# Kernel optimization log

Hardware: AMD Instinct MI355X
Metric: run time of the kernel (lower is better)

The kernel has to match this reference:

```python
import jax, jax.numpy as jnp
import numpy as np

B, T, D = 8, 2048, 1024   # batch, seq_len (== block_size), n_embed
HS = 128                   # head_size

def setup_inputs() -> dict:
    key = jax.random.key(0)
    kx, kk, kq, kv = jax.random.split(key, 4)
    s = D ** -0.5  # torch Linear default init scale ~ U(-1/sqrt(in), 1/sqrt(in))
    x  = jax.random.normal(kx, (B, T, D), dtype=jnp.float32)
    Wk = jax.random.uniform(kk, (HS, D), jnp.float32, -s, s)
    Wq = jax.random.uniform(kq, (HS, D), jnp.float32, -s, s)
    Wv = jax.random.uniform(kv, (HS, D), jnp.float32, -s, s)
    return {"x": x, "Wk": Wk, "Wq": Wq, "Wv": Wv}

def reference(x, Wk, Wq, Wv):
    # single-head causal self-attention; dropout disabled (eval mode)
    Tlen = x.shape[1]
    k = jnp.einsum('btd,hd->bth', x, Wk)   # [B,T,HS]
    q = jnp.einsum('btd,hd->bth', x, Wq)
    v = jnp.einsum('btd,hd->bth', x, Wv)
    scale = Wk.shape[0] ** -0.5
    scores = jnp.einsum('bth,bsh->bts', q, k) * scale   # [B,T,T]
    causal = jnp.tril(jnp.ones((Tlen, Tlen), dtype=bool))
    scores = jnp.where(causal, scores, -jnp.inf)
    weights = jax.nn.softmax(scores, axis=-1)
    out = jnp.einsum('bts,bsh->bth', weights, v)        # [B,T,HS]
    return out
```

## Files before the change

### kernel.cpp

```cpp
#include <hip/hip_runtime.h>
#include <hip/hip_bf16.h>
#include <math.h>

#define BATCH_N 8
#define SEQ_T   2048
#define DIM_D   1024
#define HS_N    128

using bf16x8_t = __attribute__((ext_vector_type(8))) __bf16;
using bf16x4_t = __attribute__((ext_vector_type(4))) __bf16;
using f32x4_t  = __attribute__((ext_vector_type(4))) float;

__device__ __forceinline__ f32x4_t mfma_16x16x32(bf16x8_t a, bf16x8_t b, f32x4_t c) {
  return __builtin_amdgcn_mfma_f32_16x16x32_bf16(a, b, c, 0, 0, 0);
}

__device__ __forceinline__ void async_cp16(const void* g, void* l) {
  __builtin_amdgcn_global_load_lds(
      (const __attribute__((address_space(1))) unsigned int*)g,
      (__attribute__((address_space(3))) unsigned int*)l, 16, 0, 0);
}

#define BAR()      __builtin_amdgcn_s_barrier()
#define FENCE()    asm volatile("" ::: "memory")
#define WAIT_VM(n) asm volatile("s_waitcnt vmcnt(" #n ")" ::: "memory")
#define WAIT_LGKM0 asm volatile("s_waitcnt lgkmcnt(0)" ::: "memory")

__global__ __launch_bounds__(256) void castw_kernel(
    const float* __restrict__ Wk, const float* __restrict__ Wq,
    const float* __restrict__ Wv, __bf16* __restrict__ Wb,
    unsigned int* __restrict__ km) {
  if (blockIdx.x == 0 && threadIdx.x < 8) km[threadIdx.x] = 0u;
  int idx = blockIdx.x * 256 + threadIdx.x;
  int e   = idx * 4;
  int row = e >> 10;
  int col = e & 1023;
  const float* src;
  float sc = 1.0f;
  if (row < 128) {
    src = Wk + row * DIM_D + col;
  } else if (row < 256) {
    src = Wq + (row - 128) * DIM_D + col;
    sc  = 0.08838834764831845f;
  } else {
    src = Wv + (row - 256) * DIM_D + col;
  }
  float4 v = *(const float4*)src;
  bf16x4_t o;
  o[0] = (__bf16)(v.x * sc); o[1] = (__bf16)(v.y * sc);
  o[2] = (__bf16)(v.z * sc); o[3] = (__bf16)(v.w * sc);
  *(bf16x4_t*)(Wb + e) = o;
}

__global__ __launch_bounds__(512, 2) void proj_kernel(
    const float* __restrict__ x, const __bf16* __restrict__ Wb,
    __bf16* __restrict__ Qb, __bf16* __restrict__ Kb, __bf16* __restrict__ Vt,
    unsigned int* __restrict__ km) {
  __shared__ __align__(16) char psmem[65536];

  const int tid  = threadIdx.x;
  const int lane = tid & 63;
  const int wave = tid >> 6;
  const int h    = wave >> 2;
  const int g    = wave & 3;
  const int lr = lane & 15;
  const int lq = lane >> 4;
  const int m0 = blockIdx.x * 64;

  f32x4_t acc[2][6];
  #pragma unroll
  for (int mt = 0; mt < 2; ++mt)
    #pragma unroll
    for (int nt = 0; nt < 6; ++nt) acc[mt][nt] = (f32x4_t){0.f, 0.f, 0.f, 0.f};

  auto stageA = [&](int kt) {
    char* As = psmem + (kt & 1) * 8192;
    const int r = wave * 8 + (lane >> 3);
    const int c = (lane & 7) ^ ((lane >> 3) & 7);
    async_cp16(x + (size_t)(m0 + r) * DIM_D + kt * 32 + c * 4,
               As + wave * 1024);
  };

  auto stageB = [&](int kt) {
    __bf16* Bs = (__bf16*)(psmem + 16384 + (kt & 1) * 24576);
    #pragma unroll
    for (int c = wave; c < 24; c += 8) {
      const int row = c * 16 + (lane >> 2);
      const int u   = (lane & 3) ^ ((row >> 1) & 3);
      async_cp16(Wb + (size_t)row * DIM_D + kt * 32 + u * 8, Bs + c * 512);
    }
  };

  stageA(0);
  stageB(0);

  for (int kt = 0; kt < 32; ++kt) {
    if (kt + 1 < 32) {
      stageA(kt + 1);
      stageB(kt + 1);
      WAIT_VM(4);
    } else {
      WAIT_VM(0);
    }
    BAR();
    FENCE();

    const float*  As = (const float*)(psmem + (kt & 1) * 8192);
    const __bf16* Bs = (const __bf16*)(psmem + 16384 + (kt & 1) * 24576);

    bf16x8_t af[2];
    #pragma unroll
    for (int mt = 0; mt < 2; ++mt) {
      const int ml = h * 32 + mt * 16 + lr;
      const int u0 = (lq * 2)     ^ (ml & 7);
      const int u1 = (lq * 2 + 1) ^ (ml & 7);
      f32x4_t lo = *(const f32x4_t*)(As + ml * 32 + u0 * 4);
      f32x4_t hi = *(const f32x4_t*)(As + ml * 32 + u1 * 4);
      bf16x8_t a;
      a[0] = (__bf16)lo[0]; a[1] = (__bf16)lo[1];
      a[2] = (__bf16)lo[2]; a[3] = (__bf16)lo[3];
      a[4] = (__bf16)hi[0]; a[5] = (__bf16)hi[1];
      a[6] = (__bf16)hi[2]; a[7] = (__bf16)hi[3];
      af[mt] = a;
    }
    bf16x8_t bfv[6];
    #pragma unroll
    for (int nt = 0; nt < 6; ++nt) {
      const int nl = g * 96 + nt * 16 + lr;
      bfv[nt] = *(const bf16x8_t*)(&Bs[nl * 32 + ((lq ^ ((nl >> 1) & 3)) * 8)]);
    }
    #pragma unroll
    for (int mt = 0; mt < 2; ++mt)
      #pragma unroll
      for (int nt = 0; nt < 6; ++nt)
        acc[mt][nt] = mfma_16x16x32(af[mt], bfv[nt], acc[mt][nt]);
    WAIT_LGKM0;
    BAR();
    FENCE();
  }

  __syncthreads();
  float* rowss = (float*)psmem;
  if (tid < 64) rowss[tid] = 0.f;
  __syncthreads();
  if (g < 2) {
    #pragma unroll
    for (int mt = 0; mt < 2; ++mt)
      #pragma unroll
      for (int r = 0; r < 4; ++r) {
        float s = 0.f;
        #pragma unroll
        for (int nt = 0; nt < 6; ++nt)
          if (g == 0 || nt < 2) s += acc[mt][nt][r] * acc[mt][nt][r];
        s += __shfl_xor(s, 1); s += __shfl_xor(s, 2);
        s += __shfl_xor(s, 4); s += __shfl_xor(s, 8);
        if (lr == 0) atomicAdd(&rowss[h * 32 + mt * 16 + lq * 4 + r], s);
      }
  }
  __syncthreads();
  if (tid < 64) {
    float v = rowss[tid];
    #pragma unroll
    for (int off = 1; off < 64; off <<= 1) v = fmaxf(v, __shfl_xor(v, off));
    if (tid == 0) atomicMax(km + (m0 >> 11), __float_as_uint(v));
  }

  #pragma unroll
  for (int mt = 0; mt < 2; ++mt) {
    const int t0 = m0 + h * 32 + mt * 16 + lq * 4;
    #pragma unroll
    for (int nt = 0; nt < 6; ++nt) {
      const int nn = g * 96 + nt * 16 + lr;
      if (nn < 256) {
        __bf16* dst = (nn < 128) ? (Kb + nn) : (Qb + (nn - 128));
        #pragma unroll
        for (int r = 0; r < 4; ++r)
          dst[(size_t)(t0 + r) * HS_N] = (__bf16)acc[mt][nt][r];
      } else {
        const int bb = t0 >> 11;
        const int tl = t0 & 2047;
        bf16x4_t o;
        #pragma unroll
        for (int r = 0; r < 4; ++r) o[r] = (__bf16)acc[mt][nt][r];
        *(bf16x4_t*)(Vt + (size_t)bb * (HS_N * SEQ_T) + (size_t)(nn - 256) * SEQ_T + tl) = o;
      }
    }
  }
}

__global__ __launch_bounds__(256, 2) void attn_kernel(
    const __bf16* __restrict__ Qb, const __bf16* __restrict__ Kb,
    const __bf16* __restrict__ Vt, const unsigned int* __restrict__ km,
    __bf16* __restrict__ Opart, float* __restrict__ lpart) {
  __shared__ __align__(16) char smem[81920];
  __bf16* KsBase = (__bf16*)smem;
  __bf16* VsBase = (__bf16*)(smem + 32768);
  float*  Ofl    = (float*)smem;

  const int lane = threadIdx.x & 63;
  const int wave = threadIdx.x >> 6;
  const int lr = lane & 15;
  const int lq = lane >> 4;
  const int bid  = blockIdx.x;
  const int b    = bid & 7;
  const int rest = bid >> 3;
  const int jg   = 15 - (rest >> 2);
  const int p4   = rest & 3;
  const int Q0   = jg * 128;
  const int qa   = Q0 + wave * 32;
  const int ch   = 2 * (jg + 1);
  const int c0   = (p4 * ch) >> 2;
  const int c1   = ((p4 + 1) * ch) >> 2;

  const __bf16* Qbb = Qb + (size_t)b * (SEQ_T * HS_N);
  const __bf16* Kbb = Kb + (size_t)b * (SEQ_T * HS_N);
  const __bf16* Vbb = Vt + (size_t)b * (HS_N * SEQ_T);
  __bf16* pbA = (__bf16*)(smem + 65536 + wave * 4096);
  __bf16* pbB = (__bf16*)(smem + 65536 + wave * 4096 + 2048);

  bf16x8_t qf[2][4];
  #pragma unroll
  for (int t = 0; t < 2; ++t)
    #pragma unroll
    for (int ks = 0; ks < 4; ++ks)
      qf[t][ks] = *(const bf16x8_t*)(Qbb + (size_t)(qa + t * 16 + lr) * HS_N
                                     + ks * 32 + lq * 8);

  const float km2 = __uint_as_float(km[b]);
  float mrow[2][4];
  #pragma unroll
  for (int t = 0; t < 2; ++t) {
    float qn2 = 0.f;
    #pragma unroll
    for (int ks = 0; ks < 4; ++ks)
      #pragma unroll
      for (int j = 0; j < 8; ++j) { float f = (float)qf[t][ks][j]; qn2 += f * f; }
    qn2 += __shfl_xor(qn2, 16);
    qn2 += __shfl_xor(qn2, 32);
    #pragma unroll
    for (int r2 = 0; r2 < 4; ++r2)
      mrow[t][r2] = sqrtf(__shfl(qn2, lq * 4 + r2) * km2);
  }

  f32x4_t Oa[2][8];
  #pragma unroll
  for (int t = 0; t < 2; ++t)
    #pragma unroll
    for (int o = 0; o < 8; ++o) Oa[t][o] = (f32x4_t){0.f, 0.f, 0.f, 0.f};
  float lsum[2][4] = {{0.f,0.f,0.f,0.f},{0.f,0.f,0.f,0.f}};

  auto stage = [&](int bufi, int c) {
    const int kk = c * 64;
    __bf16* Ks = KsBase + bufi * 8192;
    for (int idx = wave; idx < 32; idx += 4) {
      if (idx < 16) {
        const int row = idx * 4 + (lane >> 4);
        const int u   = (lane & 15) ^ (row & 15);
        async_cp16(Kbb + (size_t)(kk + row) * HS_N + u * 8, Ks + idx * 512);
      } else {
        const int i2  = idx - 16;
        const int row = i2 * 8 + (lane >> 3);
        const int u   = (lane & 7) ^ (row & 7);
        async_cp16(Vbb + (size_t)row * SEQ_T + kk + u * 8, VsBase + bufi * 8192 + i2 * 512);
      }
    }
  };

  if (c0 < c1) stage(0, c0);
  __syncthreads();

  for (int c = c0; c < c1; ++c) {
    const int cur = (c - c0) & 1;
    if (c + 1 < c1) {
      stage(cur ^ 1, c + 1);
      WAIT_VM(8);
    } else {
      WAIT_VM(0);
    }
    BAR();
    FENCE();

    const int kk = c * 64;
    const __bf16* Ks = KsBase + cur * 8192;
    const __bf16* Vs = VsBase + cur * 8192;

    f32x4_t s0[4], s1[4];
    #pragma unroll
    for (int nt = 0; nt < 4; ++nt) {
      s0[nt] = (f32x4_t){0.f, 0.f, 0.f, 0.f};
      s1[nt] = (f32x4_t){0.f, 0.f, 0.f, 0.f};
    }
    #pragma unroll
    for (int ks = 0; ks < 4; ++ks)
      #pragma unroll
      for (int nt = 0; nt < 4; ++nt) {
        bf16x8_t kf = *(const bf16x8_t*)(
            &Ks[(nt * 16 + lr) * 128 + (((ks * 4 + lq) ^ lr) * 8)]);
        s0[nt] = mfma_16x16x32(qf[0][ks], kf, s0[nt]);
        s1[nt] = mfma_16x16x32(qf[1][ks], kf, s1[nt]);
      }
    const int q0a = qa, q0b = qa + 16;
    if (kk + 63 > q0a) {
      #pragma unroll
      for (int nt = 0; nt < 4; ++nt) {
        const int col = kk + nt * 16 + lr;
        #pragma unroll
        for (int r2 = 0; r2 < 4; ++r2)
          if (col > q0a + lq * 4 + r2) s0[nt][r2] = -INFINITY;
      }
    }
    if (kk + 63 > q0b) {
      #pragma unroll
      for (int nt = 0; nt < 4; ++nt) {
        const int col = kk + nt * 16 + lr;
        #pragma unroll
        for (int r2 = 0; r2 < 4; ++r2)
          if (col > q0b + lq * 4 + r2) s1[nt][r2] = -INFINITY;
      }
    }

    #pragma unroll
    for (int r2 = 0; r2 < 4; ++r2) {
      float a0 = __expf(s0[0][r2] - mrow[0][r2]);
      float a1 = __expf(s0[1][r2] - mrow[0][r2]);
      float a2 = __expf(s0[2][r2] - mrow[0][r2]);
      float a3 = __expf(s0[3][r2] - mrow[0][r2]);
      s0[0][r2] = a0; s0[1][r2] = a1; s0[2][r2] = a2; s0[3][r2] = a3;
      lsum[0][r2] += (a0 + a1) + (a2 + a3);
      float b0 = __expf(s1[0][r2] - mrow[1][r2]);
      float b1 = __expf(s1[1][r2] - mrow[1][r2]);
      float b2 = __expf(s1[2][r2] - mrow[1][r2]);
      float b3 = __expf(s1[3][r2] - mrow[1][r2]);
      s1[0][r2] = b0; s1[1][r2] = b1; s1[2][r2] = b2; s1[3][r2] = b3;
      lsum[1][r2] += (b0 + b1) + (b2 + b3);
    }

    #pragma unroll
    for (int nt = 0; nt < 4; ++nt)
      #pragma unroll
      for (int r2 = 0; r2 < 4; ++r2) {
        const int prow = lq * 4 + r2;
        const int pcol = (nt * 16 + lr) ^ ((prow & 7) << 3);
        pbA[prow * 64 + pcol] = (__bf16)s0[nt][r2];
        pbB[prow * 64 + pcol] = (__bf16)s1[nt][r2];
      }

    #pragma unroll
    for (int k2 = 0; k2 < 2; ++k2) {
      const int au = ((k2 * 4 + lq) ^ (lr & 7)) << 3;
      bf16x8_t afrA = *(const bf16x8_t*)(pbA + lr * 64 + au);
      bf16x8_t afrB = *(const bf16x8_t*)(pbB + lr * 64 + au);
      #pragma unroll
      for (int o = 0; o < 8; ++o) {
        bf16x8_t vfr = *(const bf16x8_t*)(
            &Vs[(o * 16 + lr) * 64 + (((k2 * 4 + lq) ^ (lr & 7)) * 8)]);
        Oa[0][o] = mfma_16x16x32(afrA, vfr, Oa[0][o]);
        Oa[1][o] = mfma_16x16x32(afrB, vfr, Oa[1][o]);
      }
    }
    WAIT_LGKM0;
    BAR();
    FENCE();
  }

  #pragma unroll
  for (int t = 0; t < 2; ++t)
    #pragma unroll
    for (int r2 = 0; r2 < 4; ++r2) {
      float v = lsum[t][r2];
      v += __shfl_xor(v, 1);
      v += __shfl_xor(v, 2);
      v += __shfl_xor(v, 4);
      v += __shfl_xor(v, 8);
      if (lr == 0)
        lpart[bid * 128 + wave * 32 + t * 16 + lq * 4 + r2] = v;
    }

  #pragma unroll
  for (int t = 0; t < 2; ++t)
    #pragma unroll
    for (int o = 0; o < 8; ++o)
      #pragma unroll
      for (int r2 = 0; r2 < 4; ++r2)
        Ofl[(wave * 32 + t * 16 + lq * 4 + r2) * 132 + o * 16 + lr] = Oa[t][o][r2];
  __syncthreads();

  {
    const int row = threadIdx.x >> 1;
    const int cb  = (threadIdx.x & 1) * 64;
    __bf16* dst = Opart + ((size_t)bid * 128 + row) * 128 + cb;
    #pragma unroll
    for (int g2 = 0; g2 < 16; ++g2) {
      float4 f = *(const float4*)(&Ofl[row * 132 + cb + g2 * 4]);
      bf16x4_t o;
      o[0] = (__bf16)f.x; o[1] = (__bf16)f.y; o[2] = (__bf16)f.z; o[3] = (__bf16)f.w;
      *(bf16x4_t*)(dst + g2 * 4) = o;
    }
  }
}

__global__ __launch_bounds__(256) void merge_kernel(
    const __bf16* __restrict__ Opart, const float* __restrict__ lpart,
    float* __restrict__ out) {
  const int idx = blockIdx.x * 256 + threadIdx.x;
  const int row = idx >> 5;
  const int c4  = (idx & 31) * 4;
  const int b   = row >> 11;
  const int tl  = row & 2047;
  const int jg  = tl >> 7;
  const int lrow = tl & 127;
  const int rbase = (15 - jg) * 4;
  float a0 = 0.f, a1 = 0.f, a2 = 0.f, a3 = 0.f, l = 0.f;
  #pragma unroll
  for (int p = 0; p < 4; ++p) {
    const int s = b + 8 * (rbase + p);
    bf16x4_t a = *(const bf16x4_t*)(Opart + ((size_t)s * 128 + lrow) * 128 + c4);
    a0 += (float)a[0]; a1 += (float)a[1]; a2 += (float)a[2]; a3 += (float)a[3];
    l += lpart[s * 128 + lrow];
  }
  const float inv = 1.0f / l;
  float4 o;
  o.x = a0 * inv; o.y = a1 * inv; o.z = a2 * inv; o.w = a3 * inv;
  *(float4*)(out + (size_t)row * HS_N + c4) = o;
}

extern "C" void kernel_launch(void* const* d_in, const int* in_sizes, int n_in,
                              void* d_out, int out_size, void* d_ws, size_t ws_size,
                              hipStream_t stream) {
  const float* x  = (const float*)d_in[0];
  const float* Wk = (const float*)d_in[1];
  const float* Wq = (const float*)d_in[2];
  const float* Wv = (const float*)d_in[3];
  float* out = (float*)d_out;

  char* ws = (char*)d_ws;
  __bf16* Wb = (__bf16*)ws;
  __bf16* Qb = (__bf16*)(ws + 786432);
  __bf16* Kb = (__bf16*)(ws + 786432 + 4194304);
  __bf16* Vt = (__bf16*)(ws + 786432 + 8388608);
  unsigned int* km = (unsigned int*)(ws + 13369344);
  __bf16* Opart = (__bf16*)(ws + 13369600);
  float*  lpart = (float*)(ws + 30146816);

  castw_kernel<<<384, 256, 0, stream>>>(Wk, Wq, Wv, Wb, km);
  proj_kernel<<<256, 512, 0, stream>>>(x, Wb, Qb, Kb, Vt, km);
  attn_kernel<<<512, 256, 0, stream>>>(Qb, Kb, Vt, km, Opart, lpart);
  merge_kernel<<<2048, 256, 0, stream>>>(Opart, lpart, out);
}
```

Measured before the change: 159.1 us.

## Load projection weights directly into registers from a K-panel layout

New measurement: 165.7 us. 4.2% more time.

```diff
diff --git a/kernel.cpp b/kernel.cpp
--- a/kernel.cpp
+++ b/kernel.cpp
@@ -25,10 +25,11 @@
 #define FENCE()    asm volatile("" ::: "memory")
 #define WAIT_VM(n) asm volatile("s_waitcnt vmcnt(" #n ")" ::: "memory")
 #define WAIT_LGKM0 asm volatile("s_waitcnt lgkmcnt(0)" ::: "memory")
+#define SCHEDBAR() __builtin_amdgcn_sched_barrier(0)
 
 __global__ __launch_bounds__(256) void castw_kernel(
     const float* __restrict__ Wk, const float* __restrict__ Wq,
-    const float* __restrict__ Wv, __bf16* __restrict__ Wb,
+    const float* __restrict__ Wv, __bf16* __restrict__ WbT,
     unsigned int* __restrict__ km) {
   if (blockIdx.x == 0 && threadIdx.x < 8) km[threadIdx.x] = 0u;
   int idx = blockIdx.x * 256 + threadIdx.x;
@@ -49,14 +50,16 @@
   bf16x4_t o;
   o[0] = (__bf16)(v.x * sc); o[1] = (__bf16)(v.y * sc);
   o[2] = (__bf16)(v.z * sc); o[3] = (__bf16)(v.w * sc);
-  *(bf16x4_t*)(Wb + e) = o;
-}
-
-__global__ __launch_bounds__(512, 2) void proj_kernel(
-    const float* __restrict__ x, const __bf16* __restrict__ Wb,
+  const int pnl = col >> 5;
+  const int c   = col & 31;
+  *(bf16x4_t*)(WbT + (size_t)pnl * 12288 + row * 32 + c) = o;
+}
+
+__global__ __launch_bounds__(512, 1) void proj_kernel(
+    const float* __restrict__ x, const __bf16* __restrict__ WbT,
     __bf16* __restrict__ Qb, __bf16* __restrict__ Kb, __bf16* __restrict__ Vt,
     unsigned int* __restrict__ km) {
-  __shared__ __align__(16) char psmem[65536];
+  __shared__ __align__(16) char psmem[16384];
 
   const int tid  = threadIdx.x;
   const int lane = tid & 63;
@@ -81,63 +84,74 @@
                As + wave * 1024);
   };
 
-  auto stageB = [&](int kt) {
-    __bf16* Bs = (__bf16*)(psmem + 16384 + (kt & 1) * 24576);
-    #pragma unroll
-    for (int c = wave; c < 24; c += 8) {
-      const int row = c * 16 + (lane >> 2);
-      const int u   = (lane & 3) ^ ((row >> 1) & 3);
-      async_cp16(Wb + (size_t)row * DIM_D + kt * 32 + u * 8, Bs + c * 512);
-    }
-  };
+  const __bf16* bp[6];
+  #pragma unroll
+  for (int nt = 0; nt < 6; ++nt)
+    bp[nt] = WbT + (size_t)(g * 96 + nt * 16 + lr) * 32 + lq * 8;
+
+  bf16x8_t bqA[6], bqB[6];
+
+#define LOADB(kt, bq)                                                   \
+  {                                                                     \
+    _Pragma("unroll")                                                   \
+    for (int nt = 0; nt < 6; ++nt) {                                    \
+      const __bf16* p_ = bp[nt] + (size_t)(kt) * 12288;                 \
+      asm volatile("global_load_dwordx4 %0, %1, off"                    \
+                   : "=&v"(bq[nt]) : "v"(p_));                          \
+    }                                                                   \
+  }
+
+#define KSTEP(kt, bqCur, bqNxt)                                         \
+  {                                                                     \
+    if ((kt) + 1 < 32) {                                                \
+      stageA((kt) + 1);                                                 \
+      LOADB((kt) + 1, bqNxt);                                           \
+      FENCE();                                                          \
+      WAIT_VM(7);                                                       \
+    } else {                                                            \
+      WAIT_VM(0);                                                       \
+    }                                                                   \
+    BAR();                                                              \
+    FENCE();                                                            \
+    SCHEDBAR();                                                         \
+    const float* As = (const float*)(psmem + ((kt) & 1) * 8192);        \
+    bf16x8_t af[2];                                                     \
+    _Pragma("unroll")                                                   \
+    for (int mt = 0; mt < 2; ++mt) {                                    \
+      const int ml = h * 32 + mt * 16 + lr;                             \
+      const int u0 = (lq * 2) ^ (ml & 7);                               \
+      const int u1 = (lq * 2 + 1) ^ (ml & 7);                           \
+      f32x4_t lo = *(const f32x4_t*)(As + ml * 32 + u0 * 4);            \
+      f32x4_t hi = *(const f32x4_t*)(As + ml * 32 + u1 * 4);            \
+      bf16x8_t a;                                                       \
+      a[0] = (__bf16)lo[0]; a[1] = (__bf16)lo[1];                       \
+      a[2] = (__bf16)lo[2]; a[3] = (__bf16)lo[3];                       \
+      a[4] = (__bf16)hi[0]; a[5] = (__bf16)hi[1];                       \
+      a[6] = (__bf16)hi[2]; a[7] = (__bf16)hi[3];                       \
+      af[mt] = a;                                                       \
+    }                                                                   \
+    _Pragma("unroll")                                                   \
+    for (int mt = 0; mt < 2; ++mt)                                      \
+      _Pragma("unroll")                                                 \
+      for (int nt = 0; nt < 6; ++nt)                                    \
+        acc[mt][nt] = mfma_16x16x32(af[mt], bqCur[nt], acc[mt][nt]);    \
+    WAIT_LGKM0;                                                         \
+    BAR();                                                              \
+    FENCE();                                                            \
+  }
 
   stageA(0);
-  stageB(0);
-
-  for (int kt = 0; kt < 32; ++kt) {
-    if (kt + 1 < 32) {
-      stageA(kt + 1);
-      stageB(kt + 1);
-      WAIT_VM(4);
-    } else {
-      WAIT_VM(0);
-    }
-    BAR();
-    FENCE();
-
-    const float*  As = (const float*)(psmem + (kt & 1) * 8192);
-    const __bf16* Bs = (const __bf16*)(psmem + 16384 + (kt & 1) * 24576);
-
-    bf16x8_t af[2];
-    #pragma unroll
-    for (int mt = 0; mt < 2; ++mt) {
-      const int ml = h * 32 + mt * 16 + lr;
-      const int u0 = (lq * 2)     ^ (ml & 7);
-      const int u1 = (lq * 2 + 1) ^ (ml & 7);
-      f32x4_t lo = *(const f32x4_t*)(As + ml * 32 + u0 * 4);
-      f32x4_t hi = *(const f32x4_t*)(As + ml * 32 + u1 * 4);
-      bf16x8_t a;
-      a[0] = (__bf16)lo[0]; a[1] = (__bf16)lo[1];
-      a[2] = (__bf16)lo[2]; a[3] = (__bf16)lo[3];
-      a[4] = (__bf16)hi[0]; a[5] = (__bf16)hi[1];
-      a[6] = (__bf16)hi[2]; a[7] = (__bf16)hi[3];
-      af[mt] = a;
-    }
-    bf16x8_t bfv[6];
-    #pragma unroll
-    for (int nt = 0; nt < 6; ++nt) {
-      const int nl = g * 96 + nt * 16 + lr;
-      bfv[nt] = *(const bf16x8_t*)(&Bs[nl * 32 + ((lq ^ ((nl >> 1) & 3)) * 8)]);
-    }
-    #pragma unroll
-    for (int mt = 0; mt < 2; ++mt)
-      #pragma unroll
-      for (int nt = 0; nt < 6; ++nt)
-        acc[mt][nt] = mfma_16x16x32(af[mt], bfv[nt], acc[mt][nt]);
-    WAIT_LGKM0;
-    BAR();
-    FENCE();
-  }
+  LOADB(0, bqA);
+  FENCE();
+
+  #pragma unroll 1
+  for (int kt2 = 0; kt2 < 16; ++kt2) {
+    const int kt = kt2 * 2;
+    KSTEP(kt,     bqA, bqB);
+    KSTEP(kt + 1, bqB, bqA);
+  }
+#undef KSTEP
+#undef LOADB
 
   __syncthreads();
   float* rowss = (float*)psmem;
@@ -434,7 +448,7 @@
   float* out = (float*)d_out;
 
   char* ws = (char*)d_ws;
-  __bf16* Wb = (__bf16*)ws;
+  __bf16* WbT = (__bf16*)ws;
   __bf16* Qb = (__bf16*)(ws + 786432);
   __bf16* Kb = (__bf16*)(ws + 786432 + 4194304);
   __bf16* Vt = (__bf16*)(ws + 786432 + 8388608);
@@ -442,8 +456,8 @@
   __bf16* Opart = (__bf16*)(ws + 13369600);
   float*  lpart = (float*)(ws + 30146816);
 
-  castw_kernel<<<384, 256, 0, stream>>>(Wk, Wq, Wv, Wb, km);
-  proj_kernel<<<256, 512, 0, stream>>>(x, Wb, Qb, Kb, Vt, km);
+  castw_kernel<<<384, 256, 0, stream>>>(Wk, Wq, Wv, WbT, km);
+  proj_kernel<<<256, 512, 0, stream>>>(x, WbT, Qb, Kb, Vt, km);
   attn_kernel<<<512, 256, 0, stream>>>(Qb, Kb, Vt, km, Opart, lpart);
   merge_kernel<<<2048, 256, 0, stream>>>(Opart, lpart, out);
 }
```
